# Kernel optimization log

Hardware: AMD Instinct MI355X
Metric: run time of the kernel (lower is better)

The kernel has to match this reference:

```python
import jax, jax.numpy as jnp
import numpy as np

T, B, I, H = 512, 128, 256, 512
HX = H + I


def setup_inputs() -> dict:
    key = jax.random.key(0)
    ks = jax.random.split(key, 9)
    s_hx = 1.0 / np.sqrt(HX)
    return {
        "x": jax.random.normal(ks[0], (T, B, I), dtype=jnp.float32),
        "Wf": jax.random.uniform(ks[1], (HX, H), jnp.float32, -s_hx, s_hx),
        "bf": jax.random.uniform(ks[2], (H,), jnp.float32, -s_hx, s_hx),
        "Wi": jax.random.uniform(ks[3], (HX, H), jnp.float32, -s_hx, s_hx),
        "bi": jax.random.uniform(ks[4], (H,), jnp.float32, -s_hx, s_hx),
        "Wc": jax.random.uniform(ks[5], (HX, H), jnp.float32, -s_hx, s_hx),
        "bc": jax.random.uniform(ks[6], (H,), jnp.float32, -s_hx, s_hx),
        "Wo": jax.random.uniform(ks[7], (HX, H), jnp.float32, -s_hx, s_hx),
        "bo": jax.random.uniform(ks[8], (H,), jnp.float32, -s_hx, s_hx),
    }


def reference(x, Wf, bf, Wi, bi, Wc, bc, Wo, bo):
    # x: [T, B, I]; returns stacked hidden states [T, B, H]
    B_, H_ = x.shape[1], Wf.shape[1]
    h0 = jnp.zeros((B_, H_), dtype=x.dtype)
    C0 = jnp.zeros((B_, H_), dtype=x.dtype)

    def step(carry, x_t):
        h, C = carry
        hx = jnp.concatenate([h, x_t], axis=1)  # [B, H+I]
        ft = jax.nn.sigmoid(hx @ Wf + bf)
        it = jax.nn.sigmoid(hx @ Wi + bi)
        C = ft * C + it * jnp.tanh(hx @ Wc + bc)
        o = jax.nn.sigmoid(hx @ Wo + bo)
        h = o * jnp.tanh(C)
        return (h, C), h

    _, hs = jax.lax.scan(step, (h0, C0), x)
    return hs
```

## Files before the change

kernel.cpp:

```cpp
#include <hip/hip_runtime.h>
#include <math.h>

#define T_STEPS 512
#define B_SZ    128
#define I_SZ    256
#define H_SZ    512
#define HX_SZ   768
#define NG      2048
#define KB_H    16
#define KB_X    8
#define KB_TOT  24
#define W_ELEMS (HX_SZ * NG)
#define NWG     256
#define BH      (B_SZ * H_SZ)
#define BI      (B_SZ * I_SZ)
#define NFLAG   128

typedef __attribute__((ext_vector_type(8))) short bf16x8;
typedef __attribute__((ext_vector_type(4))) short bf16x4;
typedef __attribute__((ext_vector_type(4))) float f32x4;

__device__ __forceinline__ unsigned short f2bf_rne(float f) {
    unsigned u = __builtin_bit_cast(unsigned, f);
    unsigned r = u + 0x7fffu + ((u >> 16) & 1u);
    return (unsigned short)(r >> 16);
}
__device__ __forceinline__ float bf2f(unsigned short h) {
    unsigned u = ((unsigned)h) << 16;
    return __builtin_bit_cast(float, u);
}
__device__ __forceinline__ float fast_tanh(float x) {
    x = fminf(15.f, fmaxf(-15.f, x));
    const float e = __expf(2.f * x);
    return (e - 1.f) / (e + 1.f);
}

__global__ __launch_bounds__(256) void repack_frag(
    const float* __restrict__ Wf, const float* __restrict__ Wi,
    const float* __restrict__ Wc, const float* __restrict__ Wo,
    unsigned short* __restrict__ Whi, unsigned short* __restrict__ Wlo)
{
    int id = blockIdx.x * 256 + threadIdx.x;
    int j    = id & 7;
    int lane = (id >> 3) & 63;
    int fkb  = (id >> 9);
    int kb   = fkb % KB_TOT;
    int ng   = fkb / KB_TOT;
    int n = ng * 16 + (lane & 15);
    int k = kb * 32 + (lane >> 4) * 8 + j;
    int g  = n & 3;
    int jh = n >> 2;
    const float* Ws = (g == 0) ? Wf : (g == 1) ? Wi : (g == 2) ? Wc : Wo;
    float w = Ws[k * H_SZ + jh];
    unsigned short wh = f2bf_rne(w);
    unsigned short wl = f2bf_rne(w - bf2f(wh));
    Whi[id] = wh;
    Wlo[id] = wl;
}

__global__ __launch_bounds__(256) void pack_bias(
    const float* __restrict__ bf, const float* __restrict__ bi,
    const float* __restrict__ bc, const float* __restrict__ bo,
    float* __restrict__ bpk, unsigned int* __restrict__ tok)
{
    int c = blockIdx.x * 256 + threadIdx.x;
    if (c < 8 * NFLAG) tok[(size_t)c * 16] = 0u;
    int jh = c >> 2, g = c & 3;
    const float* bs = (g == 0) ? bf : (g == 1) ? bi : (g == 2) ? bc : bo;
    bpk[c] = bs[jh];
}

__global__ __launch_bounds__(256, 1) void lstm_persist(
    const float* __restrict__ x_all,
    const unsigned short* __restrict__ Whi,
    const unsigned short* __restrict__ Wlo,
    const float* __restrict__ bpk,
    float* __restrict__ out,
    unsigned short* __restrict__ hhi,
    unsigned short* __restrict__ hlo,
    unsigned int* __restrict__ tok)
{
    __shared__ __align__(16) unsigned short sh_hi[16 * 512];
    __shared__ __align__(16) unsigned short sh_lo[16 * 512];
    __shared__ __align__(16) unsigned short sx_hi[16 * 256];
    __shared__ __align__(16) unsigned short sx_lo[16 * 256];
    __shared__ float preact[16][64];

    const int tid  = threadIdx.x;
    const int lane = tid & 63;
    const int wv   = tid >> 6;
    const int w    = blockIdx.x;
    const int xcd  = w & 7;
    const int q    = w >> 3;
    const int bt   = q & 7;
    const int ngg  = xcd * 4 + (q >> 3);
    const int ng   = ngg * 4 + wv;
    const int b0   = bt * 16;
    const int mrow = lane & 15;
    const int quad = lane >> 4;
    unsigned int* const gflags = tok + (size_t)bt * (NFLAG * 16);
    unsigned int* const myflag = gflags + (size_t)(ngg * 4 + wv) * 16;

    bf16x8 wh[KB_TOT], wl[KB_TOT];
    {
        const bf16x8* __restrict__ Wh8 = (const bf16x8*)Whi;
        const bf16x8* __restrict__ Wl8 = (const bf16x8*)Wlo;
        const int wbase = ng * KB_TOT * 64 + lane;
        #pragma unroll
        for (int kb = 0; kb < KB_TOT; ++kb) {
            wh[kb] = Wh8[wbase + kb * 64];
            wl[kb] = Wl8[wbase + kb * 64];
        }
    }
    #pragma unroll
    for (int kb = 0; kb < KB_TOT; ++kb) {
        asm volatile("" : "+v"(wh[kb]));
        asm volatile("" : "+v"(wl[kb]));
    }

    const int bl = tid >> 4;
    const int jl = tid & 15;
    const int pidx = (b0 + bl) * H_SZ + ngg * 16 + jl;
    const f32x4 bias = ((const f32x4*)bpk)[ngg * 16 + jl];
    float Creg = 0.f;

    int hgo[4], xgo[4], hlds[4], xlds[4];
    #pragma unroll
    for (int r = 0; r < 4; ++r) {
        const int row = r * 4 + wv;
        hgo[r]  = (b0 + row) * H_SZ + lane * 8;
        hlds[r] = (row * 512 + lane * 8) ^ ((row & 15) << 3);
        xgo[r]  = (b0 + row) * I_SZ + lane * 4;
        xlds[r] = (row * 256 + lane * 4) ^ ((row & 15) << 3);
    }
    const int hfr = mrow * 512 + quad * 8;
    const int xfr = mrow * 256 + quad * 8;
    const int swz = (mrow & 15) << 3;

    f32x4 xpre[4];
    #pragma unroll
    for (int r = 0; r < 4; ++r)
        xpre[r] = *(const f32x4*)(x_all + xgo[r]);

    for (int t = 0; t < T_STEPS; ++t) {
        #pragma unroll
        for (int r = 0; r < 4; ++r) {
            bf16x4 hv, lv;
            #pragma unroll
            for (int j = 0; j < 4; ++j) {
                const unsigned short hb = f2bf_rne(xpre[r][j]);
                hv[j] = (short)hb;
                lv[j] = (short)f2bf_rne(xpre[r][j] - bf2f(hb));
            }
            *(bf16x4*)&sx_hi[xlds[r]] = hv;
            *(bf16x4*)&sx_lo[xlds[r]] = lv;
        }
        __syncthreads();

        bf16x8 vh[4], vl[4];
        if (t > 0) {
            const unsigned int* f0 = gflags + (size_t)lane * 16;
            const unsigned int* f1 = gflags + (size_t)(lane + 64) * 16;
            const unsigned t0v = (unsigned)t;
            const unsigned long long wd0 = __builtin_amdgcn_s_memrealtime();
            for (;;) {
                unsigned a, b;
                asm volatile("global_load_dword %0, %1, off sc0 sc1"
                             : "=v"(a) : "v"(f0));
                asm volatile("global_load_dword %0, %1, off sc0 sc1"
                             : "=v"(b) : "v"(f1));
                asm volatile("s_waitcnt vmcnt(0)" ::: "memory");
                if (__all((a >= t0v) && (b >= t0v))) break;
                if (__builtin_amdgcn_s_memrealtime() - wd0 > 10000000ull) break;
                __builtin_amdgcn_s_sleep(1);
            }
            __builtin_amdgcn_sched_barrier(0);
            const unsigned short* __restrict__ hhp = hhi + ((t - 1) & 1) * BH;
            const unsigned short* __restrict__ hlp = hlo + ((t - 1) & 1) * BH;
            #pragma unroll
            for (int r = 0; r < 4; ++r) {
                asm volatile("global_load_dwordx4 %0, %1, off sc0 sc1"
                             : "=v"(vh[r]) : "v"(hhp + hgo[r]));
                asm volatile("global_load_dwordx4 %0, %1, off sc0 sc1"
                             : "=v"(vl[r]) : "v"(hlp + hgo[r]));
            }
            __builtin_amdgcn_sched_barrier(0);
        }

        if (t + 1 < T_STEPS) {
            const float* __restrict__ xn = x_all + (size_t)(t + 1) * BI;
            #pragma unroll
            for (int r = 0; r < 4; ++r)
                xpre[r] = *(const f32x4*)(xn + xgo[r]);
        }

        f32x4 a0 = {0.f, 0.f, 0.f, 0.f};
        f32x4 a1 = {0.f, 0.f, 0.f, 0.f};
        f32x4 a2 = {0.f, 0.f, 0.f, 0.f};
        #pragma unroll
        for (int kxb = 0; kxb < KB_X; ++kxb) {
            const int off = (xfr + kxb * 32) ^ swz;
            const bf16x8 xh = *(const bf16x8*)&sx_hi[off];
            const bf16x8 xl = *(const bf16x8*)&sx_lo[off];
            a0 = __builtin_amdgcn_mfma_f32_16x16x32_bf16(xh, wh[KB_H + kxb], a0, 0, 0, 0);
            a1 = __builtin_amdgcn_mfma_f32_16x16x32_bf16(xl, wh[KB_H + kxb], a1, 0, 0, 0);
            a2 = __builtin_amdgcn_mfma_f32_16x16x32_bf16(xh, wl[KB_H + kxb], a2, 0, 0, 0);
        }

        if (t > 0) {
            asm volatile("s_waitcnt vmcnt(0)" ::: "memory");
            __builtin_amdgcn_sched_barrier(0);
            #pragma unroll
            for (int r = 0; r < 4; ++r) {
                *(bf16x8*)&sh_hi[hlds[r]] = vh[r];
                *(bf16x8*)&sh_lo[hlds[r]] = vl[r];
            }
            __syncthreads();

            #pragma unroll
            for (int kb = 0; kb < KB_H; ++kb) {
                const int off = (hfr + kb * 32) ^ swz;
                const bf16x8 ah = *(const bf16x8*)&sh_hi[off];
                const bf16x8 al = *(const bf16x8*)&sh_lo[off];
                a0 = __builtin_amdgcn_mfma_f32_16x16x32_bf16(ah, wh[kb], a0, 0, 0, 0);
                a1 = __builtin_amdgcn_mfma_f32_16x16x32_bf16(al, wh[kb], a1, 0, 0, 0);
                a2 = __builtin_amdgcn_mfma_f32_16x16x32_bf16(ah, wl[kb], a2, 0, 0, 0);
            }
        }

        const f32x4 acc = a0 + a1 + a2;

        #pragma unroll
        for (int r = 0; r < 4; ++r)
            preact[quad * 4 + r][wv * 16 + mrow] = acc[r];
        __syncthreads();

        const f32x4 pa = *(const f32x4*)&preact[bl][jl * 4];
        const float pf = pa[0] + bias[0];
        const float pi = pa[1] + bias[1];
        const float pc = pa[2] + bias[2];
        const float po = pa[3] + bias[3];
        const float fg = 1.f / (1.f + __expf(-pf));
        const float ig = 1.f / (1.f + __expf(-pi));
        const float cb = fast_tanh(pc);
        const float og = 1.f / (1.f + __expf(-po));
        const float Cn = fg * Creg + ig * cb;
        const float hn = og * fast_tanh(Cn);
        Creg = Cn;

        const int pw = t & 1;
        const unsigned short hb16 = f2bf_rne(hn);
        const unsigned hv32 = hb16;
        const unsigned lv32 = f2bf_rne(hn - bf2f(hb16));
        {
            const unsigned short* ph = hhi + pw * BH + pidx;
            const unsigned short* pl = hlo + pw * BH + pidx;
            asm volatile("global_store_short %0, %1, off sc0 sc1"
                         :: "v"(ph), "v"(hv32) : "memory");
            asm volatile("global_store_short %0, %1, off sc0 sc1"
                         :: "v"(pl), "v"(lv32) : "memory");
            asm volatile("s_waitcnt vmcnt(0)" ::: "memory");
            if (lane == 0) {
                const unsigned fv = (unsigned)(t + 1);
                asm volatile("global_store_dword %0, %1, off sc0 sc1"
                             :: "v"(myflag), "v"(fv) : "memory");
            }
        }
        out[(size_t)t * BH + pidx] = hn;
    }
}

extern "C" void kernel_launch(void* const* d_in, const int* in_sizes, int n_in,
                              void* d_out, int out_size, void* d_ws, size_t ws_size,
                              hipStream_t stream)
{
    const float* x  = (const float*)d_in[0];
    const float* Wf = (const float*)d_in[1];
    const float* bf = (const float*)d_in[2];
    const float* Wi = (const float*)d_in[3];
    const float* bi = (const float*)d_in[4];
    const float* Wc = (const float*)d_in[5];
    const float* bc = (const float*)d_in[6];
    const float* Wo = (const float*)d_in[7];
    const float* bo = (const float*)d_in[8];
    float* out = (float*)d_out;

    unsigned short* Whi = (unsigned short*)d_ws;
    unsigned short* Wlo = Whi + W_ELEMS;
    float* bpk = (float*)(Wlo + W_ELEMS);
    unsigned short* hb = (unsigned short*)(bpk + NG);
    unsigned short* hhi = hb;
    unsigned short* hlo = hb + 2 * BH;
    unsigned int* tok = (unsigned int*)(hlo + 2 * BH);

    repack_frag<<<W_ELEMS / 256, 256, 0, stream>>>(Wf, Wi, Wc, Wo, Whi, Wlo);
    pack_bias<<<NG / 256, 256, 0, stream>>>(bf, bi, bc, bo, bpk, tok);
    lstm_persist<<<NWG, 256, 0, stream>>>(x, Whi, Wlo, bpk, out, hhi, hlo, tok);
}
```

Measured before the change: 1.856 ms.

## Replace per-wave flag barrier with epoch-tagged packed hidden-state words

Drops the separate per-wave flag array and the store-wait-flag sequence. Each hidden value is now written as one 32-bit word holding the bf16 hi part, a truncated lo part, and a 2-bit step tag. Readers poll the data words themselves until every tag matches the expected step, then unpack them into LDS. Loads for the next step are issued speculatively right after the store. This removes a global round trip and the vmcnt wait per step. In exchange the lowest 2 bits of the lo correction term are lost, and each thread reads twice as many bytes per poll.

```diff
diff --git a/kernel.cpp b/kernel.cpp
--- a/kernel.cpp
+++ b/kernel.cpp
@@ -14,11 +14,11 @@
 #define NWG     256
 #define BH      (B_SZ * H_SZ)
 #define BI      (B_SZ * I_SZ)
-#define NFLAG   128
 
 typedef __attribute__((ext_vector_type(8))) short bf16x8;
 typedef __attribute__((ext_vector_type(4))) short bf16x4;
 typedef __attribute__((ext_vector_type(4))) float f32x4;
+typedef __attribute__((ext_vector_type(4))) unsigned int u32x4;
 
 __device__ __forceinline__ unsigned short f2bf_rne(float f) {
     unsigned u = __builtin_bit_cast(unsigned, f);
@@ -61,13 +61,21 @@
 __global__ __launch_bounds__(256) void pack_bias(
     const float* __restrict__ bf, const float* __restrict__ bi,
     const float* __restrict__ bc, const float* __restrict__ bo,
-    float* __restrict__ bpk, unsigned int* __restrict__ tok)
+    float* __restrict__ bpk)
 {
     int c = blockIdx.x * 256 + threadIdx.x;
-    if (c < 8 * NFLAG) tok[(size_t)c * 16] = 0u;
     int jh = c >> 2, g = c & 3;
     const float* bs = (g == 0) ? bf : (g == 1) ? bi : (g == 2) ? bc : bo;
     bpk[c] = bs[jh];
+}
+
+__global__ __launch_bounds__(256) void init_h(unsigned int* __restrict__ hpk)
+{
+    int i = blockIdx.x * 256 + threadIdx.x;
+    const unsigned v = (i < BH) ? 1u : 0u;
+    const unsigned int* p = hpk + i;
+    asm volatile("global_store_dword %0, %1, off sc0 sc1"
+                 :: "v"(p), "v"(v) : "memory");
 }
 
 __global__ __launch_bounds__(256, 1) void lstm_persist(
@@ -76,9 +84,7 @@
     const unsigned short* __restrict__ Wlo,
     const float* __restrict__ bpk,
     float* __restrict__ out,
-    unsigned short* __restrict__ hhi,
-    unsigned short* __restrict__ hlo,
-    unsigned int* __restrict__ tok)
+    unsigned int* __restrict__ hpk)
 {
     __shared__ __align__(16) unsigned short sh_hi[16 * 512];
     __shared__ __align__(16) unsigned short sh_lo[16 * 512];
@@ -98,8 +104,6 @@
     const int b0   = bt * 16;
     const int mrow = lane & 15;
     const int quad = lane >> 4;
-    unsigned int* const gflags = tok + (size_t)bt * (NFLAG * 16);
-    unsigned int* const myflag = gflags + (size_t)(ngg * 4 + wv) * 16;
 
     bf16x8 wh[KB_TOT], wl[KB_TOT];
     {
@@ -142,6 +146,8 @@
     for (int r = 0; r < 4; ++r)
         xpre[r] = *(const f32x4*)(x_all + xgo[r]);
 
+    u32x4 smp[8];
+
     for (int t = 0; t < T_STEPS; ++t) {
         #pragma unroll
         for (int r = 0; r < 4; ++r) {
@@ -156,36 +162,6 @@
             *(bf16x4*)&sx_lo[xlds[r]] = lv;
         }
         __syncthreads();
-
-        bf16x8 vh[4], vl[4];
-        if (t > 0) {
-            const unsigned int* f0 = gflags + (size_t)lane * 16;
-            const unsigned int* f1 = gflags + (size_t)(lane + 64) * 16;
-            const unsigned t0v = (unsigned)t;
-            const unsigned long long wd0 = __builtin_amdgcn_s_memrealtime();
-            for (;;) {
-                unsigned a, b;
-                asm volatile("global_load_dword %0, %1, off sc0 sc1"
-                             : "=v"(a) : "v"(f0));
-                asm volatile("global_load_dword %0, %1, off sc0 sc1"
-                             : "=v"(b) : "v"(f1));
-                asm volatile("s_waitcnt vmcnt(0)" ::: "memory");
-                if (__all((a >= t0v) && (b >= t0v))) break;
-                if (__builtin_amdgcn_s_memrealtime() - wd0 > 10000000ull) break;
-                __builtin_amdgcn_s_sleep(1);
-            }
-            __builtin_amdgcn_sched_barrier(0);
-            const unsigned short* __restrict__ hhp = hhi + ((t - 1) & 1) * BH;
-            const unsigned short* __restrict__ hlp = hlo + ((t - 1) & 1) * BH;
-            #pragma unroll
-            for (int r = 0; r < 4; ++r) {
-                asm volatile("global_load_dwordx4 %0, %1, off sc0 sc1"
-                             : "=v"(vh[r]) : "v"(hhp + hgo[r]));
-                asm volatile("global_load_dwordx4 %0, %1, off sc0 sc1"
-                             : "=v"(vl[r]) : "v"(hlp + hgo[r]));
-            }
-            __builtin_amdgcn_sched_barrier(0);
-        }
 
         if (t + 1 < T_STEPS) {
             const float* __restrict__ xn = x_all + (size_t)(t + 1) * BI;
@@ -208,12 +184,47 @@
         }
 
         if (t > 0) {
+            const unsigned ep = (unsigned)((t - 1) & 3);
+            const unsigned int* __restrict__ hrd = hpk + ((t - 1) & 1) * BH;
             asm volatile("s_waitcnt vmcnt(0)" ::: "memory");
             __builtin_amdgcn_sched_barrier(0);
+            const unsigned long long wd0 = __builtin_amdgcn_s_memrealtime();
+            for (;;) {
+                unsigned m = 0;
+                #pragma unroll
+                for (int i = 0; i < 8; ++i) {
+                    m |= (smp[i][0] ^ ep); m |= (smp[i][1] ^ ep);
+                    m |= (smp[i][2] ^ ep); m |= (smp[i][3] ^ ep);
+                }
+                if (__all((m & 3u) == 0u)) break;
+                if (__builtin_amdgcn_s_memrealtime() - wd0 > 10000000ull) break;
+                __builtin_amdgcn_s_sleep(1);
+                #pragma unroll
+                for (int r = 0; r < 4; ++r) {
+                    asm volatile("global_load_dwordx4 %0, %1, off sc0 sc1"
+                                 : "=v"(smp[2 * r]) : "v"(hrd + hgo[r]));
+                    asm volatile("global_load_dwordx4 %0, %1, off sc0 sc1"
+                                 : "=v"(smp[2 * r + 1]) : "v"(hrd + hgo[r] + 4));
+                }
+                asm volatile("s_waitcnt vmcnt(0)" ::: "memory");
+                __builtin_amdgcn_sched_barrier(0);
+            }
+
             #pragma unroll
             for (int r = 0; r < 4; ++r) {
-                *(bf16x8*)&sh_hi[hlds[r]] = vh[r];
-                *(bf16x8*)&sh_lo[hlds[r]] = vl[r];
+                const u32x4 pa = smp[2 * r];
+                const u32x4 pb = smp[2 * r + 1];
+                u32x4 hi, lo;
+                hi[0] = (pa[0] >> 16) | (pa[1] & 0xffff0000u);
+                hi[1] = (pa[2] >> 16) | (pa[3] & 0xffff0000u);
+                hi[2] = (pb[0] >> 16) | (pb[1] & 0xffff0000u);
+                hi[3] = (pb[2] >> 16) | (pb[3] & 0xffff0000u);
+                lo[0] = (pa[0] & 0xffffu) | (pa[1] << 16);
+                lo[1] = (pa[2] & 0xffffu) | (pa[3] << 16);
+                lo[2] = (pb[0] & 0xffffu) | (pb[1] << 16);
+                lo[3] = (pb[2] & 0xffffu) | (pb[3] << 16);
+                *(u32x4*)&sh_hi[hlds[r]] = hi;
+                *(u32x4*)&sh_lo[hlds[r]] = lo;
             }
             __syncthreads();
 
@@ -248,25 +259,27 @@
         const float hn = og * fast_tanh(Cn);
         Creg = Cn;
 
-        const int pw = t & 1;
         const unsigned short hb16 = f2bf_rne(hn);
-        const unsigned hv32 = hb16;
-        const unsigned lv32 = f2bf_rne(hn - bf2f(hb16));
+        const unsigned short lb16 = f2bf_rne(hn - bf2f(hb16));
+        const unsigned wpk = ((unsigned)hb16 << 16) | ((unsigned)lb16 & 0xFFFCu)
+                           | (unsigned)(t & 3);
         {
-            const unsigned short* ph = hhi + pw * BH + pidx;
-            const unsigned short* pl = hlo + pw * BH + pidx;
-            asm volatile("global_store_short %0, %1, off sc0 sc1"
-                         :: "v"(ph), "v"(hv32) : "memory");
-            asm volatile("global_store_short %0, %1, off sc0 sc1"
-                         :: "v"(pl), "v"(lv32) : "memory");
-            asm volatile("s_waitcnt vmcnt(0)" ::: "memory");
-            if (lane == 0) {
-                const unsigned fv = (unsigned)(t + 1);
-                asm volatile("global_store_dword %0, %1, off sc0 sc1"
-                             :: "v"(myflag), "v"(fv) : "memory");
-            }
+            const unsigned int* ph = hpk + (t & 1) * BH + pidx;
+            asm volatile("global_store_dword %0, %1, off sc0 sc1"
+                         :: "v"(ph), "v"(wpk) : "memory");
         }
         out[(size_t)t * BH + pidx] = hn;
+
+        if (t + 1 < T_STEPS) {
+            const unsigned int* __restrict__ hnx = hpk + (t & 1) * BH;
+            #pragma unroll
+            for (int r = 0; r < 4; ++r) {
+                asm volatile("global_load_dwordx4 %0, %1, off sc0 sc1"
+                             : "=v"(smp[2 * r]) : "v"(hnx + hgo[r]));
+                asm volatile("global_load_dwordx4 %0, %1, off sc0 sc1"
+                             : "=v"(smp[2 * r + 1]) : "v"(hnx + hgo[r] + 4));
+            }
+        }
     }
 }
 
@@ -288,12 +301,10 @@
     unsigned short* Whi = (unsigned short*)d_ws;
     unsigned short* Wlo = Whi + W_ELEMS;
     float* bpk = (float*)(Wlo + W_ELEMS);
-    unsigned short* hb = (unsigned short*)(bpk + NG);
-    unsigned short* hhi = hb;
-    unsigned short* hlo = hb + 2 * BH;
-    unsigned int* tok = (unsigned int*)(hlo + 2 * BH);
+    unsigned int* hpk = (unsigned int*)(bpk + NG);
 
     repack_frag<<<W_ELEMS / 256, 256, 0, stream>>>(Wf, Wi, Wc, Wo, Whi, Wlo);
-    pack_bias<<<NG / 256, 256, 0, stream>>>(bf, bi, bc, bo, bpk, tok);
-    lstm_persist<<<NWG, 256, 0, stream>>>(x, Whi, Wlo, bpk, out, hhi, hlo, tok);
-}
+    pack_bias<<<NG / 256, 256, 0, stream>>>(bf, bi, bc, bo, bpk);
+    init_h<<<2 * BH / 256, 256, 0, stream>>>(hpk);
+    lstm_persist<<<NWG, 256, 0, stream>>>(x, Whi, Wlo, bpk, out, hpk);
+}
```

Result: slower. 2.354 ms (+26.9%).
